# Optimization experiments

Hardware: AMD Instinct MI355X
Metric: run time of the kernel (lower is better)

The kernel has to match this reference:

```python
import jax, jax.numpy as jnp
import numpy as np

D_MODEL = 1024
N_HEADS = 16
D_HEAD = D_MODEL // N_HEADS
RANK = 128
N_COMPRESS = 64
STATE_DIM = 64
B_SZ = 2
S_LEN = 2048


def setup_inputs() -> dict:
    key = jax.random.key(0)
    ks = jax.random.split(key, 12)
    x = jax.random.normal(ks[0], (B_SZ, S_LEN, D_MODEL), dtype=jnp.float32)
    A = jax.random.normal(ks[1], (STATE_DIM, STATE_DIM), dtype=jnp.float32) * 0.01
    B_ssm = jax.random.normal(ks[2], (D_MODEL, STATE_DIM), dtype=jnp.float32) * 0.01
    W_imp = jax.random.normal(ks[3], (D_MODEL, STATE_DIM), dtype=jnp.float32) * 0.02   # Linear(state_dim->d_model), weight [out,in]
    W_router = jax.random.normal(ks[4], (N_COMPRESS, D_MODEL), dtype=jnp.float32) * 0.02
    compress_neurons = jax.random.normal(ks[5], (N_COMPRESS, D_MODEL, RANK), dtype=jnp.float32) * 0.02
    Wq = jax.random.normal(ks[6], (D_MODEL, RANK), dtype=jnp.float32) * 0.02
    Wk = jax.random.normal(ks[7], (D_MODEL, RANK), dtype=jnp.float32) * 0.02
    Wv = jax.random.normal(ks[8], (D_MODEL, RANK), dtype=jnp.float32) * 0.02
    Wo = jax.random.normal(ks[9], (D_MODEL, D_MODEL), dtype=jnp.float32) * 0.02
    mask = jnp.tril(jnp.ones((S_LEN, S_LEN), dtype=bool))[None, None]  # [1,1,S,S] causal
    return {"x": x, "A": A, "B_ssm": B_ssm, "W_imp": W_imp, "W_router": W_router,
            "compress_neurons": compress_neurons, "Wq": Wq, "Wk": Wk, "Wv": Wv,
            "Wo": Wo, "mask": mask}


def reference(x, A, B_ssm, W_imp, W_router, compress_neurons, Wq, Wk, Wv, Wo, mask):
    Bn, S, D = x.shape
    # ---- SSM: h_t = h_{t-1} @ A + x_t @ B (only final state is used) ----
    xB = jnp.einsum('bsd,dn->bsn', x, B_ssm)  # precompute input projection

    def step(h, u):
        h = h @ A + u
        return h, None

    h0 = jnp.zeros((Bn, STATE_DIM), dtype=x.dtype)
    h_final, _ = jax.lax.scan(step, h0, jnp.swapaxes(xB, 0, 1))  # scan over S

    h_proj = h_final @ W_imp.T                       # [B, d_model]
    importance = jax.nn.softmax(jnp.einsum('bsd,bd->bs', x, h_proj), axis=-1)

    # ---- Routing ----
    token_pref = jax.nn.softmax(x @ W_router.T, axis=-1)          # [B,S,n_compress]
    nw = jnp.einsum('bs,bsn->bn', importance, token_pref)         # [B,n_compress]
    nw = nw / (nw.sum(axis=-1, keepdims=True) + 1e-8)

    # ---- Shared compression -> QKV ----
    shared_compress = jnp.einsum('bn,ndr->bdr', nw, compress_neurons)  # [B,D,rank]
    hcomp = jnp.einsum('bsd,bdr->bsr', x, shared_compress)             # [B,S,rank]
    Q = (hcomp @ Wq.T).reshape(Bn, S, N_HEADS, D_HEAD).transpose(0, 2, 1, 3)
    K = (hcomp @ Wk.T).reshape(Bn, S, N_HEADS, D_HEAD).transpose(0, 2, 1, 3)
    V = (hcomp @ Wv.T).reshape(Bn, S, N_HEADS, D_HEAD).transpose(0, 2, 1, 3)

    scores = jnp.einsum('bhqd,bhkd->bhqk', Q, K) / np.sqrt(D_HEAD).astype(x.dtype)
    scores = jnp.where(mask, scores, jnp.array(-jnp.inf, dtype=scores.dtype))
    attn = jax.nn.softmax(scores, axis=-1)
    attn_out = jnp.einsum('bhqk,bhkd->bhqd', attn, V)
    attn_out = attn_out.transpose(0, 2, 1, 3).reshape(Bn, S, D_MODEL)
    output = attn_out @ Wo.T
    return output
```

## Files before the change

### kernel.cpp

```cpp
#include <hip/hip_runtime.h>
#include <hip/hip_bf16.h>

typedef __bf16 bf16x8 __attribute__((ext_vector_type(8)));
typedef float  f32x4  __attribute__((ext_vector_type(4)));
typedef float  f32x16 __attribute__((ext_vector_type(16)));
typedef unsigned int uint4v __attribute__((ext_vector_type(4)));

__device__ __forceinline__ unsigned short f2bf(float f){
  union { float f; unsigned int u; } v; v.f = f;
  unsigned int r = (v.u + 0x7FFFu + ((v.u >> 16) & 1u)) >> 16;
  return (unsigned short)r;
}

__device__ __forceinline__ float bf2f(unsigned short u){
  union { unsigned int i; float f; } v; v.i = ((unsigned int)u) << 16; return v.f;
}

__device__ __forceinline__ unsigned pkbf(float a, float b){
  unsigned r;
  asm("v_cvt_pk_bf16_f32 %0, %1, %2" : "=v"(r) : "v"(a), "v"(b));
  return r;
}

__device__ __forceinline__ void gload_lds16(const void* g, void* l){
  __builtin_amdgcn_global_load_lds(
      (const __attribute__((address_space(1))) unsigned int*)g,
      (__attribute__((address_space(3))) unsigned int*)l, 16, 0, 0);
}

#define MFMA16(a,b,c) __builtin_amdgcn_mfma_f32_16x16x32_bf16((a),(b),(c),0,0,0)
#define MFMA32(a,b,c) __builtin_amdgcn_mfma_f32_32x32x16_bf16((a),(b),(c),0,0,0)

__global__ void k_conv_x(const float* __restrict__ x, unsigned short* __restrict__ o){
  int i = (blockIdx.x * 256 + threadIdx.x) * 4;
  float4 v = *reinterpret_cast<const float4*>(x + i);
  ushort4 r; r.x = f2bf(v.x); r.y = f2bf(v.y); r.z = f2bf(v.z); r.w = f2bf(v.w);
  *reinterpret_cast<ushort4*>(o + i) = r;
}

__global__ void k_conv_w(const float* __restrict__ Wq, const float* __restrict__ Wk,
                         const float* __restrict__ Wv, const float* __restrict__ Wo,
                         const float* __restrict__ Wr,
                         unsigned short* __restrict__ wqkv, unsigned short* __restrict__ wo,
                         unsigned short* __restrict__ wrt){
  int j = (blockIdx.x * 256 + threadIdx.x) * 4;
  if (j < 393216){
    const float* s;
    if (j < 131072) s = Wq + j; else if (j < 262144) s = Wk + (j - 131072); else s = Wv + (j - 262144);
    float4 v = *reinterpret_cast<const float4*>(s);
    ushort4 r; r.x = f2bf(v.x); r.y = f2bf(v.y); r.z = f2bf(v.z); r.w = f2bf(v.w);
    *reinterpret_cast<ushort4*>(wqkv + j) = r;
  } else if (j < 1441792){
    int jj = j - 393216;
    float4 v = *reinterpret_cast<const float4*>(Wo + jj);
    ushort4 r; r.x = f2bf(v.x); r.y = f2bf(v.y); r.z = f2bf(v.z); r.w = f2bf(v.w);
    *reinterpret_cast<ushort4*>(wo + jj) = r;
  } else {
    int jj = j - 1441792;
    int n = jj >> 10, d = jj & 1023;
    ushort4 r;
    if (n < 64){
      float4 v = *reinterpret_cast<const float4*>(Wr + n * 1024 + d);
      r.x = f2bf(v.x); r.y = f2bf(v.y); r.z = f2bf(v.z); r.w = f2bf(v.w);
    } else { r.x = 0; r.y = 0; r.z = 0; r.w = 0; }
    *reinterpret_cast<ushort4*>(wrt + jj) = r;
  }
}

template<int CBF16>
__global__ __launch_bounds__(256) void k_gemm(
    const unsigned short* __restrict__ A, const unsigned short* __restrict__ Bt,
    void* __restrict__ Cv, int M, int N, int K,
    long sA, long sB, long sC)
{
  __shared__ __align__(16) unsigned short Al[128 * 64];
  __shared__ __align__(16) unsigned short Bl[128 * 64];
  const int tid = threadIdx.x, wv = tid >> 6, lane = tid & 63;
  const int bm = blockIdx.y * 128, bn = blockIdx.x * 128, z = blockIdx.z;
  const unsigned short* Ab = A + (long)z * sA;
  const unsigned short* Bb = Bt + (long)z * sB;
  const f32x4 zero = {0.f, 0.f, 0.f, 0.f};
  f32x4 acc[4][4];
  #pragma unroll
  for (int i = 0; i < 4; ++i)
    #pragma unroll
    for (int j = 0; j < 4; ++j) acc[i][j] = zero;
  const int mo = (wv & 1) * 64, no = (wv >> 1) * 64;

  for (int k0 = 0; k0 < K; k0 += 64){
    __syncthreads();
    #pragma unroll
    for (int i = 0; i < 4; ++i){
      int rr = (wv * 4 + i) * 8 + (lane >> 3);
      gload_lds16(Ab + (long)(bm + rr) * K + k0 + (lane & 7) * 8, &Al[(wv * 4 + i) * 8 * 64]);
      gload_lds16(Bb + (long)(bn + rr) * K + k0 + (lane & 7) * 8, &Bl[(wv * 4 + i) * 8 * 64]);
    }
    __syncthreads();
    #pragma unroll
    for (int ks = 0; ks < 2; ++ks){
      bf16x8 af[4], bfr[4];
      #pragma unroll
      for (int mi = 0; mi < 4; ++mi)
        af[mi] = *reinterpret_cast<const bf16x8*>(&Al[(mo + mi * 16 + (lane & 15)) * 64 + ks * 32 + (lane >> 4) * 8]);
      #pragma unroll
      for (int ni = 0; ni < 4; ++ni)
        bfr[ni] = *reinterpret_cast<const bf16x8*>(&Bl[(no + ni * 16 + (lane & 15)) * 64 + ks * 32 + (lane >> 4) * 8]);
      #pragma unroll
      for (int mi = 0; mi < 4; ++mi)
        #pragma unroll
        for (int ni = 0; ni < 4; ++ni)
          acc[mi][ni] = MFMA16(af[mi], bfr[ni], acc[mi][ni]);
    }
  }

  #pragma unroll
  for (int mi = 0; mi < 4; ++mi)
    #pragma unroll
    for (int ni = 0; ni < 4; ++ni)
      #pragma unroll
      for (int r = 0; r < 4; ++r){
        int row = bm + mo + mi * 16 + (lane >> 4) * 4 + r;
        int col = bn + no + ni * 16 + (lane & 15);
        float v = acc[mi][ni][r];
        if (CBF16) ((unsigned short*)Cv)[(long)z * sC + (long)row * N + col] = f2bf(v);
        else       ((float*)Cv)[(long)z * sC + (long)row * N + col] = v;
      }
}

__global__ __launch_bounds__(256) void k_gemm64(
    const unsigned short* __restrict__ A, const unsigned short* __restrict__ Bt,
    float* __restrict__ C, int M, int N, int K)
{
  __shared__ __align__(16) unsigned short Al[128 * 64];
  __shared__ __align__(16) unsigned short Bl[64 * 64];
  const int tid = threadIdx.x, wv = tid >> 6, lane = tid & 63;
  const int bm = blockIdx.y * 128, bn = blockIdx.x * 64;
  const f32x4 zero = {0.f, 0.f, 0.f, 0.f};
  f32x4 acc[4][2];
  #pragma unroll
  for (int i = 0; i < 4; ++i){ acc[i][0] = zero; acc[i][1] = zero; }
  const int mo = (wv & 1) * 64, no = (wv >> 1) * 32;

  for (int k0 = 0; k0 < K; k0 += 64){
    __syncthreads();
    #pragma unroll
    for (int i = 0; i < 4; ++i){
      int rr = (wv * 4 + i) * 8 + (lane >> 3);
      gload_lds16(A + (long)(bm + rr) * K + k0 + (lane & 7) * 8, &Al[(wv * 4 + i) * 8 * 64]);
    }
    #pragma unroll
    for (int i = 0; i < 2; ++i){
      int rr = (wv * 2 + i) * 8 + (lane >> 3);
      gload_lds16(Bt + (long)(bn + rr) * K + k0 + (lane & 7) * 8, &Bl[(wv * 2 + i) * 8 * 64]);
    }
    __syncthreads();
    #pragma unroll
    for (int ks = 0; ks < 2; ++ks){
      bf16x8 af[4], bfr[2];
      #pragma unroll
      for (int mi = 0; mi < 4; ++mi)
        af[mi] = *reinterpret_cast<const bf16x8*>(&Al[(mo + mi * 16 + (lane & 15)) * 64 + ks * 32 + (lane >> 4) * 8]);
      #pragma unroll
      for (int ni = 0; ni < 2; ++ni)
        bfr[ni] = *reinterpret_cast<const bf16x8*>(&Bl[(no + ni * 16 + (lane & 15)) * 64 + ks * 32 + (lane >> 4) * 8]);
      #pragma unroll
      for (int mi = 0; mi < 4; ++mi)
        #pragma unroll
        for (int ni = 0; ni < 2; ++ni)
          acc[mi][ni] = MFMA16(af[mi], bfr[ni], acc[mi][ni]);
    }
  }

  #pragma unroll
  for (int mi = 0; mi < 4; ++mi)
    #pragma unroll
    for (int ni = 0; ni < 2; ++ni)
      #pragma unroll
      for (int r = 0; r < 4; ++r){
        int row = bm + mo + mi * 16 + (lane >> 4) * 4 + r;
        int col = bn + no + ni * 16 + (lane & 15);
        C[(long)row * N + col] = acc[mi][ni][r];
      }
}

__global__ __launch_bounds__(256) void k_gemmsk(
    const unsigned short* __restrict__ A, const unsigned short* __restrict__ Bt,
    float* __restrict__ P, int M, int N, int Kfull, int KS,
    long sA, long sB)
{
  __shared__ __align__(16) unsigned short Al[128 * 64];
  __shared__ __align__(16) unsigned short Bl[128 * 64];
  const int tid = threadIdx.x, wv = tid >> 6, lane = tid & 63;
  const int bm = blockIdx.y * 128, bn = blockIdx.x * 128, z = blockIdx.z;
  const int b = z >> 2, s = z & 3;
  const unsigned short* Ab = A + (long)b * sA;
  const unsigned short* Bb = Bt + (long)b * sB;
  float* Pb = P + (long)z * M * N;
  const f32x4 zero = {0.f, 0.f, 0.f, 0.f};
  f32x4 acc[4][4];
  #pragma unroll
  for (int i = 0; i < 4; ++i)
    #pragma unroll
    for (int j = 0; j < 4; ++j) acc[i][j] = zero;
  const int mo = (wv & 1) * 64, no = (wv >> 1) * 64;

  const int k1 = s * KS + KS;
  for (int k0 = s * KS; k0 < k1; k0 += 64){
    __syncthreads();
    #pragma unroll
    for (int i = 0; i < 4; ++i){
      int rr = (wv * 4 + i) * 8 + (lane >> 3);
      gload_lds16(Ab + (long)(bm + rr) * Kfull + k0 + (lane & 7) * 8, &Al[(wv * 4 + i) * 8 * 64]);
      gload_lds16(Bb + (long)(bn + rr) * Kfull + k0 + (lane & 7) * 8, &Bl[(wv * 4 + i) * 8 * 64]);
    }
    __syncthreads();
    #pragma unroll
    for (int ks = 0; ks < 2; ++ks){
      bf16x8 af[4], bfr[4];
      #pragma unroll
      for (int mi = 0; mi < 4; ++mi)
        af[mi] = *reinterpret_cast<const bf16x8*>(&Al[(mo + mi * 16 + (lane & 15)) * 64 + ks * 32 + (lane >> 4) * 8]);
      #pragma unroll
      for (int ni = 0; ni < 4; ++ni)
        bfr[ni] = *reinterpret_cast<const bf16x8*>(&Bl[(no + ni * 16 + (lane & 15)) * 64 + ks * 32 + (lane >> 4) * 8]);
      #pragma unroll
      for (int mi = 0; mi < 4; ++mi)
        #pragma unroll
        for (int ni = 0; ni < 4; ++ni)
          acc[mi][ni] = MFMA16(af[mi], bfr[ni], acc[mi][ni]);
    }
  }

  #pragma unroll
  for (int mi = 0; mi < 4; ++mi)
    #pragma unroll
    for (int ni = 0; ni < 4; ++ni)
      #pragma unroll
      for (int r = 0; r < 4; ++r){
        int row = bm + mo + mi * 16 + (lane >> 4) * 4 + r;
        int col = bn + no + ni * 16 + (lane & 15);
        Pb[(long)row * N + col] = acc[mi][ni][r];
      }
}

__global__ __launch_bounds__(256) void k_hred(const float* __restrict__ hpp,
                                              unsigned short* __restrict__ hcomp){
  int i4 = (blockIdx.x * 256 + threadIdx.x) * 4;
  int b = i4 >> 18;
  int rem = i4 & 262143;
  const float* p = hpp + (long)(b * 4) * 262144 + rem;
  f32x4 v = *reinterpret_cast<const f32x4*>(p);
  v += *reinterpret_cast<const f32x4*>(p + 262144);
  v += *reinterpret_cast<const f32x4*>(p + 524288);
  v += *reinterpret_cast<const f32x4*>(p + 786432);
  ushort4 o; o.x = f2bf(v[0]); o.y = f2bf(v[1]); o.z = f2bf(v[2]); o.w = f2bf(v[3]);
  *reinterpret_cast<ushort4*>(hcomp + (long)b * 262144 + rem) = o;
}

__global__ __launch_bounds__(256) void k_xbt(const float* __restrict__ x, const float* __restrict__ Bs,
                                             float* __restrict__ xbt){
  int b = blockIdx.x >> 5, t = blockIdx.x & 31;
  int tid = threadIdx.x, n = tid & 63, p = tid >> 6;
  const float* xr = x + ((long)b * 2048 + 2016 + t) * 1024 + p * 256;
  const float* Bp = Bs + (p * 256) * 64 + n;
  float a0 = 0.f, a1 = 0.f, a2 = 0.f, a3 = 0.f;
  #pragma unroll 4
  for (int d = 0; d < 256; d += 4){
    float4 xv = *reinterpret_cast<const float4*>(xr + d);
    a0 += xv.x * Bp[(d    ) * 64];
    a1 += xv.y * Bp[(d + 1) * 64];
    a2 += xv.z * Bp[(d + 2) * 64];
    a3 += xv.w * Bp[(d + 3) * 64];
  }
  __shared__ float red[4][64];
  red[p][n] = (a0 + a1) + (a2 + a3);
  __syncthreads();
  if (tid < 64){
    float s = red[0][tid] + red[1][tid] + red[2][tid] + red[3][tid];
    xbt[(b * 32 + t) * 64 + tid] = s;
  }
}

__global__ void k_scan(const float* __restrict__ xbt, const float* __restrict__ A,
                       float* __restrict__ hfin){
  int b = blockIdx.x, j = threadIdx.x;
  float Ac[64];
  #pragma unroll
  for (int i = 0; i < 64; ++i) Ac[i] = A[i * 64 + j];
  __shared__ float xs[32][64];
  __shared__ float hs[64];
  #pragma unroll
  for (int t = 0; t < 32; ++t) xs[t][j] = xbt[(b * 32 + t) * 64 + j];
  hs[j] = xs[0][j];
  __syncthreads();
  for (int t = 1; t < 32; ++t){
    float a0 = 0.f, a1 = 0.f, a2 = 0.f, a3 = 0.f;
    #pragma unroll
    for (int ii = 0; ii < 16; ++ii){
      float4 h4 = *reinterpret_cast<const float4*>(&hs[ii * 4]);
      a0 += h4.x * Ac[ii * 4 + 0];
      a1 += h4.y * Ac[ii * 4 + 1];
      a2 += h4.z * Ac[ii * 4 + 2];
      a3 += h4.w * Ac[ii * 4 + 3];
    }
    float acc = (a0 + a1) + (a2 + a3) + xs[t][j];
    __syncthreads();
    hs[j] = acc;
    __syncthreads();
  }
  hfin[b * 64 + j] = hs[j];
}

__global__ __launch_bounds__(256) void k_hproj(const float* __restrict__ hfin,
                                               const float* __restrict__ Wimp,
                                               float* __restrict__ hproj){
  int bid = blockIdx.x;
  int b = bid >> 2;
  int d = (bid & 3) * 256 + threadIdx.x;
  __shared__ float hs[64];
  if (threadIdx.x < 64) hs[threadIdx.x] = hfin[b * 64 + threadIdx.x];
  __syncthreads();
  const float* wr = Wimp + (long)d * 64;
  float a0 = 0.f, a1 = 0.f, a2 = 0.f, a3 = 0.f;
  #pragma unroll
  for (int k = 0; k < 64; k += 4){
    float4 w4 = *reinterpret_cast<const float4*>(wr + k);
    float4 h4 = *reinterpret_cast<const float4*>(&hs[k]);
    a0 += w4.x * h4.x; a1 += w4.y * h4.y; a2 += w4.z * h4.z; a3 += w4.w * h4.w;
  }
  hproj[b * 1024 + d] = (a0 + a1) + (a2 + a3);
}

__global__ void k_logits(const float* __restrict__ x, const float* __restrict__ hproj,
                         float* __restrict__ l){
  int tid = threadIdx.x, lane = tid & 63, wv = tid >> 6;
  int rowbase = blockIdx.x * 16;
  int b = rowbase >> 11;
  float hp[16];
  #pragma unroll
  for (int i = 0; i < 16; ++i) hp[i] = hproj[b * 1024 + i * 64 + lane];
  for (int rr = 0; rr < 4; ++rr){
    int row = rowbase + wv * 4 + rr;
    const float* xr = x + (long)row * 1024;
    float acc = 0.f;
    #pragma unroll
    for (int i = 0; i < 16; ++i) acc += xr[i * 64 + lane] * hp[i];
    #pragma unroll
    for (int o = 32; o; o >>= 1) acc += __shfl_xor(acc, o, 64);
    if (lane == 0) l[row] = acc;
  }
}

__global__ void k_impsm(const float* __restrict__ l, float* __restrict__ imp){
  int b = blockIdx.x, tid = threadIdx.x, lane = tid & 63, wv = tid >> 6;
  __shared__ float red[16];
  float v0 = l[b * 2048 + tid], v1 = l[b * 2048 + 1024 + tid];
  float m = fmaxf(v0, v1);
  #pragma unroll
  for (int o = 32; o; o >>= 1) m = fmaxf(m, __shfl_xor(m, o, 64));
  if (lane == 0) red[wv] = m;
  __syncthreads();
  float M = red[0];
  #pragma unroll
  for (int i = 1; i < 16; ++i) M = fmaxf(M, red[i]);
  __syncthreads();
  float e0 = __expf(v0 - M), e1 = __expf(v1 - M);
  float s = e0 + e1;
  #pragma unroll
  for (int o = 32; o; o >>= 1) s += __shfl_xor(s, o, 64);
  if (lane == 0) red[wv] = s;
  __syncthreads();
  float S = 0.f;
  #pragma unroll
  for (int i = 0; i < 16; ++i) S += red[i];
  float inv = 1.f / S;
  imp[b * 2048 + tid] = e0 * inv;
  imp[b * 2048 + 1024 + tid] = e1 * inv;
}

__global__ void k_nwpart(const float* __restrict__ rpp, const float* __restrict__ imp,
                         float* __restrict__ nwp){
  int bid = blockIdx.x; int b = bid >> 4, chunk = bid & 15;
  int tid = threadIdx.x, wv = tid >> 6, lane = tid & 63;
  float accn = 0.f;
  for (int t = 0; t < 32; ++t){
    int s = chunk * 128 + wv * 32 + t;
    long off = ((long)b * 2048 + s) * 128 + lane;
    float v = rpp[off] + rpp[off + 524288] + rpp[off + 1048576] + rpp[off + 1572864];
    float mx = v;
    #pragma unroll
    for (int o = 32; o; o >>= 1) mx = fmaxf(mx, __shfl_xor(mx, o, 64));
    float e = __expf(v - mx);
    float sm = e;
    #pragma unroll
    for (int o = 32; o; o >>= 1) sm += __shfl_xor(sm, o, 64);
    accn += imp[b * 2048 + s] * (e / sm);
  }
  __shared__ float red[4][64];
  red[wv][lane] = accn;
  __syncthreads();
  if (wv == 0){
    float t = red[0][lane] + red[1][lane] + red[2][lane] + red[3][lane];
    nwp[bid * 64 + lane] = t;
  }
}

__global__ void k_nwfin(const float* __restrict__ nwp, float* __restrict__ nw){
  int b = blockIdx.x, lane = threadIdx.x;
  float a = 0.f;
  #pragma unroll
  for (int c = 0; c < 16; ++c) a += nwp[(b * 16 + c) * 64 + lane];
  float tot = a;
  #pragma unroll
  for (int o = 32; o; o >>= 1) tot += __shfl_xor(tot, o, 64);
  nw[b * 64 + lane] = a / (tot + 1e-8f);
}

__global__ void k_sc(const float* __restrict__ cn, const float* __restrict__ nw,
                     unsigned short* __restrict__ sct){
  int tid = threadIdx.x;
  long idx = (long)blockIdx.x * 256 + tid;
  int d = (int)(idx >> 5); int r0 = (int)(idx & 31) * 4;
  __shared__ float nws[128];
  if (tid < 128) nws[tid] = nw[tid];
  __syncthreads();
  f32x4 a0 = {0.f,0.f,0.f,0.f}, a1 = {0.f,0.f,0.f,0.f};
  for (int n = 0; n < 64; ++n){
    f32x4 c = *reinterpret_cast<const f32x4*>(&cn[((long)n * 1024 + d) * 128 + r0]);
    a0 += nws[n] * c;
    a1 += nws[64 + n] * c;
  }
  #pragma unroll
  for (int e = 0; e < 4; ++e){
    sct[(long)(r0 + e) * 1024 + d]        = f2bf(a0[e]);
    sct[(long)(128 + r0 + e) * 1024 + d]  = f2bf(a1[e]);
  }
}

__global__ __launch_bounds__(256, 4) void k_attn(const unsigned short* __restrict__ qkv,
                                                 unsigned short* __restrict__ Op,
                                                 float* __restrict__ ml){
  __shared__ __align__(16) unsigned short KlA[64 * 64];
  __shared__ __align__(16) unsigned short VtA[64 * 64];
  char* Kl = (char*)KlA;
  char* Vt = (char*)VtA;
  const int tid = threadIdx.x, wq = tid >> 6, lane = tid & 63;
  const int l31 = lane & 31, hi = lane >> 5;
  const float CEXP = 0.18033688011112042f;

  int li = blockIdx.x;
  int j = li & 7, m = li >> 3;
  int g = j * 4 + (m & 3);
  int k = (m >> 2) & 7;
  int ph = m >> 5;
  int qb = (ph < 2) ? (15 - k) : k;
  int half = ph & 1;
  int h = g & 15, b = g >> 4;
  int pidx = (g * 16 + qb) * 2 + half;

  int qbase = qb * 128 + wq * 32;
  int KTw = qbase >> 6;
  const unsigned short* base = qkv + (long)b * 2048 * 3072;

  bf16x8 qf[4];
  #pragma unroll
  for (int i = 0; i < 4; ++i)
    qf[i] = *reinterpret_cast<const bf16x8*>(base + (long)(qbase + l31) * 3072 + h * 64 + i * 16 + hi * 8);

  f32x16 oacc[2];
  #pragma unroll
  for (int d = 0; d < 2; ++d)
    #pragma unroll
    for (int r = 0; r < 16; ++r) oacc[d][r] = 0.f;
  float m_r = -3.0e38f, l_r = 0.f;

  const int t0 = half ? (qb + 1) : 0;

  for (int i = 0; i <= qb; ++i){
    int kt = t0 + i;
    #pragma unroll
    for (int it = 0; it < 2; ++it){
      int key = it * 32 + wq * 8 + (lane >> 3);
      int sc = (lane & 7) ^ (key & 7);
      gload_lds16(base + (long)(kt * 64 + key) * 3072 + 1024 + h * 64 + sc * 8,
                  Kl + (it * 32 + wq * 8) * 128);
    }
    #pragma unroll
    for (int it = 0; it < 2; ++it){
      int dhg = wq + it * 4;
      uint4 vvv = *reinterpret_cast<const uint4*>(base + (long)(kt * 64 + lane) * 3072 + 2048 + h * 64 + dhg * 8);
      const unsigned short* vs = reinterpret_cast<const unsigned short*>(&vvv);
      #pragma unroll
      for (int e = 0; e < 8; ++e){
        int dh = dhg * 8 + e;
        *reinterpret_cast<unsigned short*>(Vt + dh * 128 + ((((lane >> 3) ^ (dh & 7))) << 4) + (lane & 7) * 2) = vs[e];
      }
    }
    __syncthreads();

    if (kt <= KTw){
      bool diag = (kt == KTw);

      f32x16 sa[2];
      __builtin_amdgcn_s_setprio(1);
      #pragma unroll
      for (int kb = 0; kb < 2; ++kb){
        #pragma unroll
        for (int r = 0; r < 16; ++r) sa[kb][r] = 0.f;
        int row = kb * 32 + l31;
        #pragma unroll
        for (int i2 = 0; i2 < 4; ++i2){
          bf16x8 kf = *reinterpret_cast<const bf16x8*>(
              Kl + row * 128 + ((((i2 << 1) | hi) ^ (l31 & 7)) << 4));
          sa[kb] = MFMA32(kf, qf[i2], sa[kb]);
        }
      }
      __builtin_amdgcn_s_setprio(0);

      float pv[32];
      #pragma unroll
      for (int kb = 0; kb < 2; ++kb)
        #pragma unroll
        for (int r = 0; r < 16; ++r) pv[kb * 16 + r] = sa[kb][r];

      if (diag){
        int qg = qbase + l31;
        #pragma unroll
        for (int kb = 0; kb < 2; ++kb)
          #pragma unroll
          for (int r = 0; r < 16; ++r){
            int kg = kt * 64 + kb * 32 + (r & 3) + ((r >> 2) << 3) + (hi << 2);
            if (kg > qg) pv[kb * 16 + r] = -3.0e38f;
          }
      }

      float mx = pv[0];
      #pragma unroll
      for (int r = 1; r < 32; ++r) mx = fmaxf(mx, pv[r]);
      mx = fmaxf(mx, __shfl_xor(mx, 32, 64));

      float scl;
      if (__all(mx <= m_r + 44.0f)){
        scl = 1.f;
      } else {
        float mnew = fmaxf(m_r, mx);
        scl = exp2f((m_r - mnew) * CEXP);
        m_r = mnew;
        #pragma unroll
        for (int d = 0; d < 2; ++d)
          #pragma unroll
          for (int r = 0; r < 16; ++r) oacc[d][r] *= scl;
      }
      float mn_c = m_r * CEXP;
      float rs = 0.f;
      #pragma unroll
      for (int r = 0; r < 32; ++r){
        float e = exp2f(__builtin_fmaf(pv[r], CEXP, -mn_c));
        pv[r] = e; rs += e;
      }
      rs += __shfl_xor(rs, 32, 64);
      l_r = l_r * scl + rs;

      bf16x8 pa[4];
      #pragma unroll
      for (int kb = 0; kb < 2; ++kb){
        unsigned W[4][2], X[4][2];
        #pragma unroll
        for (int u = 0; u < 4; ++u){
          W[u][0] = pkbf(pv[kb * 16 + 4 * u + 0], pv[kb * 16 + 4 * u + 1]);
          W[u][1] = pkbf(pv[kb * 16 + 4 * u + 2], pv[kb * 16 + 4 * u + 3]);
        }
        #pragma unroll
        for (int u = 0; u < 4; ++u){
          X[u][0] = (unsigned)__shfl_xor((int)W[u][0], 32, 64);
          X[u][1] = (unsigned)__shfl_xor((int)W[u][1], 32, 64);
        }
        #pragma unroll
        for (int t2 = 0; t2 < 2; ++t2){
          int u0 = 2 * t2, u1 = u0 + 1;
          uint4v wt;
          wt.x = hi ? X[u1][0] : W[u0][0];
          wt.y = hi ? X[u1][1] : W[u0][1];
          wt.z = hi ? W[u1][0] : X[u0][0];
          wt.w = hi ? W[u1][1] : X[u0][1];
          pa[kb * 2 + t2] = __builtin_bit_cast(bf16x8, wt);
        }
      }
      __builtin_amdgcn_s_setprio(1);
      #pragma unroll
      for (int db = 0; db < 2; ++db){
        int row = db * 32 + l31;
        #pragma unroll
        for (int t = 0; t < 4; ++t){
          bf16x8 vf = *reinterpret_cast<const bf16x8*>(
              Vt + row * 128 + ((((t << 1) | hi) ^ (l31 & 7)) << 4));
          oacc[db] = MFMA32(vf, pa[t], oacc[db]);
        }
      }
      __builtin_amdgcn_s_setprio(0);
    }
    __syncthreads();
  }

  unsigned short* Oq = Op + (long)pidx * 8192 + (wq * 32 + l31) * 64;
  #pragma unroll
  for (int db = 0; db < 2; ++db)
    #pragma unroll
    for (int r4 = 0; r4 < 4; ++r4){
      ushort4 o;
      o.x = f2bf(oacc[db][r4 * 4 + 0]);
      o.y = f2bf(oacc[db][r4 * 4 + 1]);
      o.z = f2bf(oacc[db][r4 * 4 + 2]);
      o.w = f2bf(oacc[db][r4 * 4 + 3]);
      *reinterpret_cast<ushort4*>(Oq + db * 32 + r4 * 8 + hi * 4) = o;
    }
  if (hi == 0){
    float2 v; v.x = m_r; v.y = l_r;
    *reinterpret_cast<float2*>(ml + ((long)pidx * 128 + wq * 32 + l31) * 2) = v;
  }
}

__global__ __launch_bounds__(256) void k_amerge(const unsigned short* __restrict__ Op,
                                                const float* __restrict__ ml,
                                                unsigned short* __restrict__ ao){
  const float CEXP = 0.18033688011112042f;
  int mid = blockIdx.x;
  int g = mid >> 4, qb = mid & 15;
  int b = g >> 4, h = g & 15;
  const unsigned short* O0 = Op + (long)mid * 2 * 8192;
  const unsigned short* O1 = O0 + 8192;
  const float* ml0 = ml + (long)mid * 2 * 256;
  const float* ml1 = ml0 + 256;
  int t = threadIdx.x;
  #pragma unroll
  for (int i = 0; i < 8; ++i){
    int idx = i * 256 + t;
    int q = idx >> 4, c4 = (idx & 15) * 4;
    float m0 = ml0[q * 2], l0 = ml0[q * 2 + 1];
    float m1 = ml1[q * 2], l1 = ml1[q * 2 + 1];
    float mm = fmaxf(m0, m1);
    float s0 = exp2f((m0 - mm) * CEXP), s1 = exp2f((m1 - mm) * CEXP);
    float linv = 1.f / (l0 * s0 + l1 * s1);
    s0 *= linv; s1 *= linv;
    ushort4 a = *reinterpret_cast<const ushort4*>(O0 + q * 64 + c4);
    ushort4 c = *reinterpret_cast<const ushort4*>(O1 + q * 64 + c4);
    ushort4 o;
    o.x = f2bf(bf2f(a.x) * s0 + bf2f(c.x) * s1);
    o.y = f2bf(bf2f(a.y) * s0 + bf2f(c.y) * s1);
    o.z = f2bf(bf2f(a.z) * s0 + bf2f(c.z) * s1);
    o.w = f2bf(bf2f(a.w) * s0 + bf2f(c.w) * s1);
    *reinterpret_cast<ushort4*>(ao + ((long)b * 2048 + qb * 128 + q) * 1024 + h * 64 + c4) = o;
  }
}

extern "C" void kernel_launch(void* const* d_in, const int* in_sizes, int n_in,
                              void* d_out, int out_size, void* d_ws, size_t ws_size,
                              hipStream_t stream){
  (void)in_sizes; (void)n_in; (void)out_size; (void)ws_size;
  const float* x    = (const float*)d_in[0];
  const float* A    = (const float*)d_in[1];
  const float* Bs   = (const float*)d_in[2];
  const float* Wimp = (const float*)d_in[3];
  const float* Wr   = (const float*)d_in[4];
  const float* cn   = (const float*)d_in[5];
  const float* Wq   = (const float*)d_in[6];
  const float* Wk   = (const float*)d_in[7];
  const float* Wv   = (const float*)d_in[8];
  const float* Wo   = (const float*)d_in[9];
  float* out = (float*)d_out;
  char* ws = (char*)d_ws;

  unsigned short* Opart = (unsigned short*)(ws + 0);
  float*          mlbuf = (float*)(ws + 16777216);
  unsigned short* xb16  = (unsigned short*)(ws + 0);
  float*          rpp   = (float*)(ws + 8388608);
  unsigned short* sct   = (unsigned short*)(ws + 16777216);
  float*          xbt   = (float*)(ws + 17301504);
  float*          hproj = (float*)(ws + 17317888);
  float*          lbuf  = (float*)(ws + 17326080);
  float*          imp   = (float*)(ws + 17342464);
  float*          nwp   = (float*)(ws + 17358848);
  float*          nw    = (float*)(ws + 17367040);
  float*          hfin  = (float*)(ws + 17368064);
  unsigned short* qkvb  = (unsigned short*)(ws + 17825792);
  float*          hpp   = (float*)(ws + 17825792);
  unsigned short* aob   = (unsigned short*)(ws + 42991616);
  unsigned short* wqkv  = (unsigned short*)(ws + 51380224);
  unsigned short* wo_t  = (unsigned short*)(ws + 52166656);
  unsigned short* wrt   = (unsigned short*)(ws + 54263808);
  unsigned short* hcomp = (unsigned short*)(ws + 54525952);

  k_conv_x<<<4096, 256, 0, stream>>>(x, xb16);
  k_conv_w<<<1536, 256, 0, stream>>>(Wq, Wk, Wv, Wo, Wr, wqkv, wo_t, wrt);
  k_gemmsk<<<dim3(1, 32, 4), 256, 0, stream>>>(xb16, wrt, rpp, 4096, 128, 1024, 256, 0, 0);
  k_xbt<<<64, 256, 0, stream>>>(x, Bs, xbt);
  k_scan<<<2, 64, 0, stream>>>(xbt, A, hfin);
  k_hproj<<<8, 256, 0, stream>>>(hfin, Wimp, hproj);
  k_logits<<<256, 256, 0, stream>>>(x, hproj, lbuf);
  k_impsm<<<2, 1024, 0, stream>>>(lbuf, imp);
  k_nwpart<<<32, 256, 0, stream>>>(rpp, imp, nwp);
  k_nwfin<<<2, 64, 0, stream>>>(nwp, nw);
  k_sc<<<128, 256, 0, stream>>>(cn, nw, sct);
  k_gemmsk<<<dim3(1, 16, 8), 256, 0, stream>>>(xb16, sct, hpp, 2048, 128, 1024, 256,
                                               2048L * 1024, 128L * 1024);
  k_hred<<<512, 256, 0, stream>>>(hpp, hcomp);
  k_gemm<1><<<dim3(24, 16, 2), 256, 0, stream>>>(hcomp, wqkv, qkvb, 2048, 3072, 128,
                                                 2048L * 128, 0, 2048L * 3072);
  k_attn<<<dim3(1024), 256, 0, stream>>>(qkvb, Opart, mlbuf);
  k_amerge<<<dim3(512), 256, 0, stream>>>(Opart, mlbuf, aob);
  k_gemm64<<<dim3(16, 32), 256, 0, stream>>>(aob, wo_t, out, 4096, 1024, 1024);
}
```

Baseline: 199.9 us.

## Double-buffer K/V tiles in attention kernel to overlap loads with MFMA

The attention kernel now keeps two LDS buffers for the K and transposed-V tiles. It prefetches the next key tile (async global-to-LDS for K, registers for V) while computing on the current one, then writes V into the other buffer after compute. This cuts the loop to one barrier per iteration and hides global load latency behind the QK and PV MFMAs. The cost is double the LDS footprint (32KB per block) and extra registers for the prefetched V, which may reduce occupancy at the 4-blocks-per-CU launch bound.

```diff
diff --git a/kernel.cpp b/kernel.cpp
--- a/kernel.cpp
+++ b/kernel.cpp
@@ -440,10 +440,8 @@
 __global__ __launch_bounds__(256, 4) void k_attn(const unsigned short* __restrict__ qkv,
                                                  unsigned short* __restrict__ Op,
                                                  float* __restrict__ ml){
-  __shared__ __align__(16) unsigned short KlA[64 * 64];
-  __shared__ __align__(16) unsigned short VtA[64 * 64];
-  char* Kl = (char*)KlA;
-  char* Vt = (char*)VtA;
+  __shared__ __align__(16) unsigned short KlA[2][64 * 64];
+  __shared__ __align__(16) unsigned short VtA[2][64 * 64];
   const int tid = threadIdx.x, wq = tid >> 6, lane = tid & 63;
   const int l31 = lane & 31, hi = lane >> 5;
   const float CEXP = 0.18033688011112042f;
@@ -462,6 +460,9 @@
   int KTw = qbase >> 6;
   const unsigned short* base = qkv + (long)b * 2048 * 3072;
 
+  const int sc8 = ((lane & 7) ^ (lane >> 3)) * 8;
+  const int kq8 = wq * 8 + (lane >> 3);
+
   bf16x8 qf[4];
   #pragma unroll
   for (int i = 0; i < 4; ++i)
@@ -476,27 +477,46 @@
 
   const int t0 = half ? (qb + 1) : 0;
 
+  {
+    #pragma unroll
+    for (int it = 0; it < 2; ++it)
+      gload_lds16(base + (long)(t0 * 64 + it * 32 + kq8) * 3072 + 1024 + h * 64 + sc8,
+                  (char*)&KlA[0][0] + (it * 32 + wq * 8) * 128);
+    uint4 v0 = *reinterpret_cast<const uint4*>(base + (long)(t0 * 64 + lane) * 3072 + 2048 + h * 64 + wq * 8);
+    uint4 v1 = *reinterpret_cast<const uint4*>(base + (long)(t0 * 64 + lane) * 3072 + 2048 + h * 64 + (wq + 4) * 8);
+    const unsigned short* vs0 = reinterpret_cast<const unsigned short*>(&v0);
+    const unsigned short* vs1 = reinterpret_cast<const unsigned short*>(&v1);
+    char* Vt0 = (char*)&VtA[0][0];
+    #pragma unroll
+    for (int e = 0; e < 8; ++e){
+      int dh0 = wq * 8 + e;
+      *reinterpret_cast<unsigned short*>(Vt0 + dh0 * 128 + ((((lane >> 3) ^ (dh0 & 7))) << 4) + (lane & 7) * 2) = vs0[e];
+      int dh1 = (wq + 4) * 8 + e;
+      *reinterpret_cast<unsigned short*>(Vt0 + dh1 * 128 + ((((lane >> 3) ^ (dh1 & 7))) << 4) + (lane & 7) * 2) = vs1[e];
+    }
+  }
+
   for (int i = 0; i <= qb; ++i){
+    int cur = i & 1;
     int kt = t0 + i;
-    #pragma unroll
-    for (int it = 0; it < 2; ++it){
-      int key = it * 32 + wq * 8 + (lane >> 3);
-      int sc = (lane & 7) ^ (key & 7);
-      gload_lds16(base + (long)(kt * 64 + key) * 3072 + 1024 + h * 64 + sc * 8,
-                  Kl + (it * 32 + wq * 8) * 128);
-    }
-    #pragma unroll
-    for (int it = 0; it < 2; ++it){
-      int dhg = wq + it * 4;
-      uint4 vvv = *reinterpret_cast<const uint4*>(base + (long)(kt * 64 + lane) * 3072 + 2048 + h * 64 + dhg * 8);
-      const unsigned short* vs = reinterpret_cast<const unsigned short*>(&vvv);
-      #pragma unroll
-      for (int e = 0; e < 8; ++e){
-        int dh = dhg * 8 + e;
-        *reinterpret_cast<unsigned short*>(Vt + dh * 128 + ((((lane >> 3) ^ (dh & 7))) << 4) + (lane & 7) * 2) = vs[e];
-      }
-    }
-    __syncthreads();
+    char* Kl = (char*)&KlA[cur][0];
+    char* Vt = (char*)&VtA[cur][0];
+    char* KlN = (char*)&KlA[cur ^ 1][0];
+    char* VtN = (char*)&VtA[cur ^ 1][0];
+    bool more = (i < qb);
+
+    __syncthreads();
+
+    uint4 nv0, nv1;
+    if (more){
+      int kn = kt + 1;
+      #pragma unroll
+      for (int it = 0; it < 2; ++it)
+        gload_lds16(base + (long)(kn * 64 + it * 32 + kq8) * 3072 + 1024 + h * 64 + sc8,
+                    KlN + (it * 32 + wq * 8) * 128);
+      nv0 = *reinterpret_cast<const uint4*>(base + (long)(kn * 64 + lane) * 3072 + 2048 + h * 64 + wq * 8);
+      nv1 = *reinterpret_cast<const uint4*>(base + (long)(kn * 64 + lane) * 3072 + 2048 + h * 64 + (wq + 4) * 8);
+    }
 
     if (kt <= KTw){
       bool diag = (kt == KTw);
@@ -599,7 +619,18 @@
       }
       __builtin_amdgcn_s_setprio(0);
     }
-    __syncthreads();
+
+    if (more){
+      const unsigned short* vs0 = reinterpret_cast<const unsigned short*>(&nv0);
+      const unsigned short* vs1 = reinterpret_cast<const unsigned short*>(&nv1);
+      #pragma unroll
+      for (int e = 0; e < 8; ++e){
+        int dh0 = wq * 8 + e;
+        *reinterpret_cast<unsigned short*>(VtN + dh0 * 128 + ((((lane >> 3) ^ (dh0 & 7))) << 4) + (lane & 7) * 2) = vs0[e];
+        int dh1 = (wq + 4) * 8 + e;
+        *reinterpret_cast<unsigned short*>(VtN + dh1 * 128 + ((((lane >> 3) ^ (dh1 & 7))) << 4) + (lane & 7) * 2) = vs1[e];
+      }
+    }
   }
 
   unsigned short* Oq = Op + (long)pidx * 8192 + (wq * 32 + l31) * 64;
```

After: 204.9 us. 1.02x slower.
